# Kernel tuning notes

Hardware: AMD Instinct MI355X
Metric: run time of the kernel (lower is better)

Reference implementation:

```python
import jax, jax.numpy as jnp
import numpy as np

N_NODES = 50000
N_GRAPHS = 64
LRELU_SLOPE = 0.2
BN_EPS = 1e-5

def _conv1d(x, w, b):
    # x: [B, C_in, L], w: [C_out, C_in, K] -> [B, C_out, L-K+1]
    y = jax.lax.conv_general_dilated(x, w, window_strides=(1,), padding='VALID',
                                     dimension_numbers=('NCH', 'OIH', 'NCH'))
    return y + b[None, :, None]

def setup_inputs() -> dict:
    key = jax.random.key(0)
    ks = jax.random.split(key, 24)
    E = 800000
    inp = {
        'global_rna': jax.random.randint(ks[0], (64, 3000), 0, 5, dtype=jnp.int32),
        'local_rna': jax.random.randint(ks[1], (64, 2998), 0, 65, dtype=jnp.int32),
        'pro_x': jax.random.normal(ks[2], (N_NODES, 33), jnp.float32),
        'edge_index': jax.random.randint(ks[3], (2, E), 0, N_NODES, dtype=jnp.int32),
        'pro_weight': jax.random.uniform(ks[4], (E,), jnp.float32),
        'pro_batch': jnp.sort(jax.random.randint(ks[5], (N_NODES,), 0, N_GRAPHS, dtype=jnp.int32)),
        'emb1': jax.random.normal(ks[6], (5, 128), jnp.float32),
        'emb2': jax.random.normal(ks[7], (65, 128), jnp.float32),
        'conv1_w': jax.random.normal(ks[8], (32, 3000, 8), jnp.float32) * 0.02,
        'conv1_b': jax.random.normal(ks[9], (32,), jnp.float32) * 0.02,
        'conv2_w': jax.random.normal(ks[10], (32, 2998, 8), jnp.float32) * 0.02,
        'conv2_b': jax.random.normal(ks[11], (32,), jnp.float32) * 0.02,
        'fc_xr_w': jax.random.normal(ks[12], (128, 3872), jnp.float32) * 0.02,
        'fc_xr_b': jax.random.normal(ks[13], (128,), jnp.float32) * 0.02,
        'gcn_w': jax.random.normal(ks[14], (33, 33), jnp.float32) * 0.1,
        'gcn_b': jax.random.normal(ks[15], (33,), jnp.float32) * 0.1,
        'bn_mean': jnp.zeros((33,), jnp.float32),
        'bn_var': jnp.ones((33,), jnp.float32),
        'bn_weight': jnp.ones((33,), jnp.float32),
        'bn_bias': jnp.zeros((33,), jnp.float32),
        'gat_wl': jax.random.normal(ks[16], (132, 33), jnp.float32) * 0.1,
        'gat_wr': jax.random.normal(ks[17], (132, 33), jnp.float32) * 0.1,
        'gat_att': jax.random.normal(ks[18], (2, 66), jnp.float32) * 0.1,
        'gat_b': jax.random.normal(ks[19], (132,), jnp.float32) * 0.1,
        'fc1_w': jax.random.normal(ks[20], (1024, 132), jnp.float32) * 0.05,
        'fc1_b': jax.random.normal(ks[21], (1024,), jnp.float32) * 0.05,
        'fc2_w': jax.random.normal(ks[22], (128, 1024), jnp.float32) * 0.05,
        'fc2_b': jax.random.normal(ks[23], (128,), jnp.float32) * 0.05,
    }
    return inp

def _forward(global_rna, local_rna, pro_x, edge_index, pro_weight, pro_batch,
             emb1, emb2, conv1_w, conv1_b, conv2_w, conv2_b, fc_xr_w, fc_xr_b,
             gcn_w, gcn_b, bn_mean, bn_var, bn_weight, bn_bias,
             gat_wl, gat_wr, gat_att, gat_b, fc1_w, fc1_b, fc2_w, fc2_b):
    # ---- RNA global branch ----
    xrg = emb1[global_rna]                       # [B, 3000, 128]
    xrg = _conv1d(xrg, conv1_w, conv1_b)         # [B, 32, 121]
    xrg = xrg.reshape(-1, 32 * 121) @ fc_xr_w.T + fc_xr_b
    # ---- RNA local branch ----
    xrl = emb2[local_rna]                        # [B, 2998, 128]
    xrl = _conv1d(xrl, conv2_w, conv2_b)         # [B, 32, 121]
    xrl = xrl.reshape(-1, 32 * 121) @ fc_xr_w.T + fc_xr_b
    # ---- protein GCNConv (with self-loops, symmetric norm, edge weights) ----
    N = pro_x.shape[0]
    loop = jnp.arange(N, dtype=edge_index.dtype)
    src = jnp.concatenate([edge_index[0], loop])
    dst = jnp.concatenate([edge_index[1], loop])
    w = jnp.concatenate([pro_weight, jnp.ones((N,), pro_weight.dtype)])
    deg = jax.ops.segment_sum(w, dst, num_segments=N)
    dinv = jnp.where(deg > 0, jax.lax.rsqrt(deg), 0.0)
    norm = dinv[src] * w * dinv[dst]
    h = pro_x @ gcn_w.T                          # [N, 33]
    xp = jax.ops.segment_sum(h[src] * norm[:, None], dst, num_segments=N) + gcn_b
    xp = jax.nn.relu(xp)
    # ---- NodeLevelBatchNorm (eval: running stats) ----
    inv = bn_weight * jax.lax.rsqrt(bn_var + BN_EPS)
    xp = xp * inv + (bn_bias - bn_mean * inv)
    # ---- GATv2Conv (heads=2, out=66, concat, self-loops, eval: no dropout) ----
    H, C = 2, 66
    xl = (xp @ gat_wl.T).reshape(N, H, C)
    xr = (xp @ gat_wr.T).reshape(N, H, C)
    e = jnp.sum(jax.nn.leaky_relu(xl[src] + xr[dst], LRELU_SLOPE) * gat_att, axis=-1)  # [E2, H]
    emax = jax.ops.segment_max(e, dst, num_segments=N)                                  # [N, H]
    a = jnp.exp(e - emax[dst])
    asum = jax.ops.segment_sum(a, dst, num_segments=N)
    alpha = a / asum[dst]                                                              # [E2, H]
    xp = jax.ops.segment_sum(xl[src] * alpha[:, :, None], dst, num_segments=N)
    xp = xp.reshape(N, H * C) + gat_b
    xp = jax.nn.relu(xp)
    # ---- global mean pool ----
    cnt = jax.ops.segment_sum(jnp.ones((N,), xp.dtype), pro_batch, num_segments=N_GRAPHS)
    xp = jax.ops.segment_sum(xp, pro_batch, num_segments=N_GRAPHS) / jnp.maximum(cnt, 1.0)[:, None]
    # ---- protein MLP head (dropout = identity in eval) ----
    xp = jax.nn.relu(xp @ fc1_w.T + fc1_b)
    xp = xp @ fc2_w.T + fc2_b
    xc_rna = 0.5 * (xrg + xrl)
    return (xc_rna, xp)

def reference(global_rna, local_rna, pro_x, edge_index, pro_weight, pro_batch,
              emb1, emb2, conv1_w, conv1_b, conv2_w, conv2_b, fc_xr_w, fc_xr_b,
              gcn_w, gcn_b, bn_mean, bn_var, bn_weight, bn_bias,
              gat_wl, gat_wr, gat_att, gat_b, fc1_w, fc1_b, fc2_w, fc2_b):
    return _forward(global_rna, local_rna, pro_x, edge_index, pro_weight, pro_batch,
                    emb1, emb2, conv1_w, conv1_b, conv2_w, conv2_b, fc_xr_w, fc_xr_b,
                    gcn_w, gcn_b, bn_mean, bn_var, bn_weight, bn_bias,
                    gat_wl, gat_wr, gat_att, gat_b, fc1_w, fc1_b, fc2_w, fc2_b)
```

## Files before the change

kernel.cpp:

```cpp
#include <hip/hip_runtime.h>

#define N_NODES 50000
#define N_EDGES 800000
#define LRELU_SLOPE 0.2f
#define BN_EPS 1e-5f

typedef unsigned int u32;
typedef unsigned long long u64;

__device__ __forceinline__ float lrelu(float x){ return fmaxf(x,0.f) + LRELU_SLOPE*fminf(x,0.f); }
__device__ __forceinline__ float bflo(u32 u){ return __uint_as_float(u<<16); }
__device__ __forceinline__ float bfhi(u32 u){ return __uint_as_float(u & 0xffff0000u); }
__device__ __forceinline__ u32 packbf(float a, float b){
  u32 ua = __float_as_uint(a); ua = (ua + 0x7fffu + ((ua>>16)&1u)) >> 16;
  u32 ub = __float_as_uint(b); ub = (ub + 0x7fffu + ((ub>>16)&1u)) >> 16;
  return ua | (ub<<16);
}
__device__ __forceinline__ float degof(u64 p){
  return (float)(p & 0xFFFFFFFFFFull) * (1.0f/67108864.0f);
}

template<int CTRL>
__device__ __forceinline__ float dppadd(float x){
  int y = __builtin_amdgcn_update_dpp(0, __float_as_int(x), CTRL, 0xF, 0xF, false);
  return x + __int_as_float(y);
}
__device__ __forceinline__ float red8(float p){
  p = dppadd<0x141>(p);
  p = dppadd<0x4E>(p);
  p = dppadd<0xB1>(p);
  return p;
}
__device__ __forceinline__ float redall(float v){
  v = dppadd<0x128>(v);
  v += __shfl_xor(v, 16, 64);
  v += __shfl_xor(v, 32, 64);
  return v;
}

__global__ __launch_bounds__(256) void k_hist(const int* __restrict__ eidx, const float* __restrict__ pw,
                                              u64* __restrict__ pk){
  int e = blockIdx.x*256 + threadIdx.x;
  if(e < N_EDGES){
    int d = eidx[N_EDGES + e];
    u64 q = (u64)(pw[e] * 67108864.f);
    atomicAdd(&pk[d], (1ull<<40) | q);
  }
}

__global__ __launch_bounds__(256) void k_scan1(const u64* __restrict__ pk, int* __restrict__ rowptr,
                                               int* __restrict__ bsum){
  __shared__ int sc[256];
  int b = blockIdx.x, t = threadIdx.x;
  int i = b*256 + t;
  int v = (i < N_NODES) ? (int)(pk[i] >> 40) : 0;
  sc[t] = v;
  __syncthreads();
  for(int off=1; off<256; off<<=1){
    int x = (t>=off)? sc[t-off] : 0;
    __syncthreads();
    sc[t] += x;
    __syncthreads();
  }
  if(i < N_NODES) rowptr[i] = sc[t] - v;
  if(t == 255) bsum[b] = sc[255];
}

__global__ __launch_bounds__(256) void k_scan2(const int* __restrict__ bsum, int* __restrict__ bbase,
                                               int* __restrict__ rowptr, int* __restrict__ gstart,
                                               int* __restrict__ gend){
  __shared__ int sc[256];
  int t = threadIdx.x;
  int v = (t < 196) ? bsum[t] : 0;
  sc[t] = v;
  __syncthreads();
  for(int off=1; off<256; off<<=1){
    int x = (t>=off)? sc[t-off] : 0;
    __syncthreads();
    sc[t] += x;
    __syncthreads();
  }
  if(t < 196) bbase[t] = sc[t] - v;
  if(t == 255) rowptr[N_NODES] = sc[255];
  if(t < 64){ gstart[t] = N_NODES; gend[t] = 0; }
}

__global__ __launch_bounds__(256) void k_scan3(int* __restrict__ rowptr, const int* __restrict__ bbase){
  int b = blockIdx.x, t = threadIdx.x;
  int i = b*256 + t;
  if(i < N_NODES) rowptr[i] += bbase[b];
}

__global__ __launch_bounds__(256) void k_scatter(const int* __restrict__ eidx, const float* __restrict__ pw,
                                                 const int* __restrict__ rowptr, int* __restrict__ fill,
                                                 const u64* __restrict__ pk, uint2* __restrict__ s_srcw,
                                                 int* __restrict__ srcs){
  int e = blockIdx.x*256 + threadIdx.x;
  if(e < N_EDGES){
    int d = eidx[N_EDGES + e];
    int s = eidx[e];
    float ge = rsqrtf(degof(pk[s]) + 1.f) * pw[e];
    int pos = rowptr[d] + atomicAdd(&fill[d], 1);
    uint2 pr; pr.x = (u32)s; pr.y = __float_as_uint(ge);
    s_srcw[pos] = pr;
    srcs[pos] = s;
  }
}

__global__ __launch_bounds__(256) void k_h(const float* __restrict__ px, const float* __restrict__ gw,
                                           u32* __restrict__ hb){
  int n = blockIdx.x*256 + threadIdx.x;
  if(n >= N_NODES) return;
  float x[33];
  #pragma unroll
  for(int k=0;k<33;k++) x[k] = px[n*33+k];
  float a[33];
  for(int c=0;c<33;c++){
    float s = 0.f;
    #pragma unroll
    for(int k=0;k<33;k++) s = fmaf(x[k], gw[c*33+k], s);
    a[c] = s;
  }
  #pragma unroll
  for(int d=0;d<16;d++) hb[(size_t)n*17 + d] = packbf(a[2*d], a[2*d+1]);
  hb[(size_t)n*17 + 16] = packbf(a[32], 0.f);
}

__global__ __launch_bounds__(256) void k_gcn(const u32* __restrict__ hb, const int* __restrict__ rowptr,
                                             const uint2* __restrict__ s_srcw,
                                             const u64* __restrict__ pk,
                                             const float* __restrict__ gcnb, const float* __restrict__ bnm,
                                             const float* __restrict__ bnv, const float* __restrict__ bnw,
                                             const float* __restrict__ bnb, float* __restrict__ xp1){
  int wave = threadIdx.x >> 6;
  int lane = threadIdx.x & 63;
  int n = blockIdx.x*4 + wave;
  if(n >= N_NODES) return;
  int l = lane & 15, g = lane >> 4;
  bool t0 = (l == 0);
  float dn = rsqrtf(degof(pk[n]) + 1.f);
  const u32* srow = hb + (size_t)n*17;
  u32 us  = srow[l];
  u32 ust = t0 ? srow[16] : 0u;
  float acc0, acc1, acct;
  if(g == 0){ acc0 = dn*bflo(us); acc1 = dn*bfhi(us); acct = dn*bflo(ust); }
  else      { acc0 = 0.f; acc1 = 0.f; acct = 0.f; }
  int rb = rowptr[n], re = rowptr[n+1];
  int j = rb;
  for(; j+8 <= re; j += 8){
    uint2 prA = s_srcw[j + g];
    uint2 prB = s_srcw[j + 4 + g];
    float geA = __uint_as_float(prA.y);
    float geB = __uint_as_float(prB.y);
    const u32* rA = hb + (size_t)prA.x*17;
    const u32* rB = hb + (size_t)prB.x*17;
    u32 uA  = rA[l], uB = rB[l];
    u32 utA = t0 ? rA[16] : 0u;
    u32 utB = t0 ? rB[16] : 0u;
    acc0 = fmaf(geA, bflo(uA),  fmaf(geB, bflo(uB),  acc0));
    acc1 = fmaf(geA, bfhi(uA),  fmaf(geB, bfhi(uB),  acc1));
    acct = fmaf(geA, bflo(utA), fmaf(geB, bflo(utB), acct));
  }
  if(j+4 <= re){
    uint2 pr = s_srcw[j + g];
    float ge = __uint_as_float(pr.y);
    const u32* r = hb + (size_t)pr.x*17;
    u32 u  = r[l];
    u32 ut = t0 ? r[16] : 0u;
    acc0 = fmaf(ge, bflo(u),  acc0);
    acc1 = fmaf(ge, bfhi(u),  acc1);
    acct = fmaf(ge, bflo(ut), acct);
    j += 4;
  }
  int rem = re - j;
  if(rem > 0){
    bool val = (g < rem);
    uint2 pr = s_srcw[val ? (j + g) : j];
    float ge = val ? __uint_as_float(pr.y) : 0.f;
    const u32* r = hb + (size_t)pr.x*17;
    u32 u  = r[l];
    u32 ut = t0 ? r[16] : 0u;
    acc0 = fmaf(ge, bflo(u),  acc0);
    acc1 = fmaf(ge, bfhi(u),  acc1);
    acct = fmaf(ge, bflo(ut), acct);
  }
  #pragma unroll
  for(int m=16;m<=32;m<<=1){
    acc0 += __shfl_xor(acc0, m, 64);
    acc1 += __shfl_xor(acc1, m, 64);
    acct += __shfl_xor(acct, m, 64);
  }
  if(g == 0){
    int c0 = 2*l, c1 = 2*l+1;
    float v0 = fmaxf(dn*acc0 + gcnb[c0], 0.f);
    float v1 = fmaxf(dn*acc1 + gcnb[c1], 0.f);
    float i0 = bnw[c0] / sqrtf(bnv[c0] + BN_EPS);
    float i1 = bnw[c1] / sqrtf(bnv[c1] + BN_EPS);
    float2 o;
    o.x = v0*i0 + (bnb[c0] - bnm[c0]*i0);
    o.y = v1*i1 + (bnb[c1] - bnm[c1]*i1);
    ((float2*)(xp1 + (size_t)n*36))[l] = o;
    if(t0){
      float vt = fmaxf(dn*acct + gcnb[32], 0.f);
      float it = bnw[32] / sqrtf(bnv[32] + BN_EPS);
      float2 ot; ot.x = vt*it + (bnb[32] - bnm[32]*it); ot.y = 0.f;
      ((float2*)(xp1 + (size_t)n*36))[16] = ot;
      float2 z; z.x = 0.f; z.y = 0.f;
      ((float2*)(xp1 + (size_t)n*36))[17] = z;
    }
  }
}

__global__ __launch_bounds__(320) void k_gatlin(const float* __restrict__ xp1, const float* __restrict__ wl,
                                                const float* __restrict__ wr, const float* __restrict__ att,
                                                u32* __restrict__ xlb, float* __restrict__ xr){
  __shared__ float sx[64*36];
  __shared__ float swle[66*33];
  __shared__ float swlo[66*33];
  __shared__ float swre[66*33];
  __shared__ float swro[66*33];
  __shared__ float su[2][33];
  int t = threadIdx.x;
  int n0 = blockIdx.x*64;
  int nn = N_NODES - n0; if(nn > 64) nn = 64;
  for(int i=t;i<2178;i+=320){
    int d = i/33, k = i - d*33;
    int gb = d*66 + k;
    swle[i] = wl[gb];
    swlo[i] = wl[gb+33];
    swre[i] = wr[gb];
    swro[i] = wr[gb+33];
  }
  int xcnt = nn*36;
  for(int i=t;i<xcnt;i+=320) sx[i] = xp1[(size_t)n0*36 + i];
  __syncthreads();
  if(t < 66){
    int hh = (t >= 33) ? 1 : 0;
    int k = t - 33*hh;
    float s = 0.f;
    const float* ah = att + hh*66;
    #pragma unroll 3
    for(int dd=0;dd<33;dd++){
      int p = hh*33 + dd;
      s = fmaf(ah[2*dd],   swle[p*33+k], s);
      s = fmaf(ah[2*dd+1], swlo[p*33+k], s);
    }
    su[hh][k] = s;
  }
  if(t < 264){
    int ng = t/66, p = t - ng*66;
    int nbase = ng*16;
    float al0[16], al1[16], ar0[16], ar1[16];
    #pragma unroll
    for(int i=0;i<16;i++){ al0[i]=0.f; al1[i]=0.f; ar0[i]=0.f; ar1[i]=0.f; }
    const float* wle = swle + p*33;
    const float* wlo = swlo + p*33;
    const float* wre = swre + p*33;
    const float* wro = swro + p*33;
    for(int k=0;k<33;k++){
      float w0 = wle[k], w1 = wlo[k], w2 = wre[k], w3 = wro[k];
      const float* xcol = sx + nbase*36 + k;
      #pragma unroll
      for(int i=0;i<16;i++){
        float x = xcol[i*36];
        al0[i] = fmaf(x, w0, al0[i]);
        al1[i] = fmaf(x, w1, al1[i]);
        ar0[i] = fmaf(x, w2, ar0[i]);
        ar1[i] = fmaf(x, w3, ar1[i]);
      }
    }
    int head = (p >= 33) ? 1 : 0;
    int dd = p - 33*head;
    #pragma unroll
    for(int i=0;i<16;i++){
      int n = nbase + i;
      if(n < nn){
        size_t nidx = (size_t)(n0 + n);
        xlb[nidx*72 + head*36 + dd] = packbf(al0[i], al1[i]);
        float2 v; v.x = ar0[i]; v.y = ar1[i];
        ((float2*)xr)[nidx*66 + p] = v;
      }
    }
  }
  __syncthreads();
  if(t < 128){
    int nl = t >> 1, hh = t & 1;
    if(nl < nn){
      const float* xv = sx + nl*36;
      float s = 0.f;
      #pragma unroll
      for(int k=0;k<33;k++) s = fmaf(su[hh][k], xv[k], s);
      xlb[(size_t)(n0 + nl)*72 + hh*36 + 33] =
        __float_as_uint(s * (LRELU_SLOPE*1.44269504089f));
    }
  }
}

__global__ __launch_bounds__(128) void k_gat(const int* __restrict__ rowptr, const int* __restrict__ srcs,
                                             const u32* __restrict__ xlb, const float* __restrict__ xr,
                                             const float* __restrict__ att, const float* __restrict__ gatb,
                                             float* __restrict__ xp2){
  const float ATT_SC = (1.f - LRELU_SLOPE) * 1.44269504089f;
  int n = blockIdx.x;
  int h = threadIdx.x >> 6;
  int lane = threadIdx.x & 63;
  int l8 = lane & 7, g8 = lane >> 3;
  bool t0 = (l8 == 0);
  bool g0 = (g8 == 0);
  const float* xrp = xr + (size_t)n*132 + h*66 + 8*l8;
  float2 x01 = ((const float2*)xrp)[0];
  float2 x23 = ((const float2*)xrp)[1];
  float2 x45 = ((const float2*)xrp)[2];
  float2 x67 = ((const float2*)xrp)[3];
  float2 xt  = t0 ? *(const float2*)(xr + (size_t)n*132 + h*66 + 64) : make_float2(0.f,0.f);
  const float* ap = att + h*66 + 8*l8;
  float2 a01 = ((const float2*)ap)[0];
  float2 a23 = ((const float2*)ap)[1];
  float2 a45 = ((const float2*)ap)[2];
  float2 a67 = ((const float2*)ap)[3];
  a01.x *= ATT_SC; a01.y *= ATT_SC; a23.x *= ATT_SC; a23.y *= ATT_SC;
  a45.x *= ATT_SC; a45.y *= ATT_SC; a67.x *= ATT_SC; a67.y *= ATT_SC;
  float2 atl = *(const float2*)(att + h*66 + 64);
  atl.x *= ATT_SC; atl.y *= ATT_SC;

  const u32* xbase = xlb + h*36;
  float v0,v1,v2,v3,v4,v5,v6,v7,w0,w1;

#define GSCORE(U, TU, P) { \
  v0=bflo(U.x); v1=bfhi(U.x); v2=bflo(U.y); v3=bfhi(U.y); \
  v4=bflo(U.z); v5=bfhi(U.z); v6=bflo(U.w); v7=bfhi(U.w); \
  w0=bflo(TU.x); w1=bfhi(TU.x); \
  float pA = __uint_as_float(TU.y), pB = 0.f; \
  pA = fmaf(fmaxf(v0+x01.x,0.f), a01.x, pA); \
  pB = fmaf(fmaxf(v1+x01.y,0.f), a01.y, pB); \
  pA = fmaf(fmaxf(v2+x23.x,0.f), a23.x, pA); \
  pB = fmaf(fmaxf(v3+x23.y,0.f), a23.y, pB); \
  pA = fmaf(fmaxf(v4+x45.x,0.f), a45.x, pA); \
  pB = fmaf(fmaxf(v5+x45.y,0.f), a45.y, pB); \
  pA = fmaf(fmaxf(v6+x67.x,0.f), a67.x, pA); \
  pB = fmaf(fmaxf(v7+x67.y,0.f), a67.y, pB); \
  pA = fmaf(fmaxf(w0+xt.x,0.f), atl.x, pA); \
  pB = fmaf(fmaxf(w1+xt.y,0.f), atl.y, pB); \
  P = red8(pA + pB); }

  const u32* srow = xbase + (size_t)n*72;
  uint4 su = ((const uint4*)srow)[l8];
  uint2 stl = t0 ? ((const uint2*)srow)[16] : make_uint2(0u,0u);
  float ps;
  GSCORE(su, stl, ps);
  float cn = -ps;
  float A0 = g0? v0 : 0.f, A1 = g0? v1 : 0.f, A2 = g0? v2 : 0.f, A3 = g0? v3 : 0.f;
  float A4 = g0? v4 : 0.f, A5 = g0? v5 : 0.f, A6 = g0? v6 : 0.f, A7 = g0? v7 : 0.f;
  float T0 = g0? w0 : 0.f, T1 = g0? w1 : 0.f;
  float asum = g0 ? 1.f : 0.f;

  int rb = rowptr[n], re = rowptr[n+1];
  int j = rb;
  for(; j+8 <= re; j += 8){
    int s = srcs[j + g8];
    const u32* r = xbase + (size_t)s*72;
    uint4 u = ((const uint4*)r)[l8];
    uint2 tu = t0 ? ((const uint2*)r)[16] : make_uint2(0u,0u);
    float p;
    GSCORE(u, tu, p);
    float a = __builtin_amdgcn_exp2f(p + cn);
    A0 = fmaf(a, v0, A0); A1 = fmaf(a, v1, A1); A2 = fmaf(a, v2, A2); A3 = fmaf(a, v3, A3);
    A4 = fmaf(a, v4, A4); A5 = fmaf(a, v5, A5); A6 = fmaf(a, v6, A6); A7 = fmaf(a, v7, A7);
    T0 = fmaf(a, w0, T0); T1 = fmaf(a, w1, T1);
    asum += a;
  }
  int rem = re - j;
  if(rem > 0){
    bool val = (g8 < rem);
    int s = val ? srcs[j + g8] : n;
    const u32* r = xbase + (size_t)s*72;
    uint4 u = ((const uint4*)r)[l8];
    uint2 tu = t0 ? ((const uint2*)r)[16] : make_uint2(0u,0u);
    float p;
    GSCORE(u, tu, p);
    float a = val ? __builtin_amdgcn_exp2f(p + cn) : 0.f;
    A0 = fmaf(a, v0, A0); A1 = fmaf(a, v1, A1); A2 = fmaf(a, v2, A2); A3 = fmaf(a, v3, A3);
    A4 = fmaf(a, v4, A4); A5 = fmaf(a, v5, A5); A6 = fmaf(a, v6, A6); A7 = fmaf(a, v7, A7);
    T0 = fmaf(a, w0, T0); T1 = fmaf(a, w1, T1);
    asum += a;
  }
#undef GSCORE

  A0 = redall(A0); A1 = redall(A1); A2 = redall(A2); A3 = redall(A3);
  A4 = redall(A4); A5 = redall(A5); A6 = redall(A6); A7 = redall(A7);
  T0 = redall(T0); T1 = redall(T1);
  asum = redall(asum);

  if(g0){
    float inv = 1.f / asum;
    const float* gp = gatb + h*66 + 8*l8;
    float2 g01 = ((const float2*)gp)[0];
    float2 g23 = ((const float2*)gp)[1];
    float2 g45 = ((const float2*)gp)[2];
    float2 g67 = ((const float2*)gp)[3];
    float* op = xp2 + (size_t)n*132 + h*66 + 8*l8;
    float2 o;
    o.x = fmaxf(fmaf(A0,inv,g01.x),0.f); o.y = fmaxf(fmaf(A1,inv,g01.y),0.f); ((float2*)op)[0] = o;
    o.x = fmaxf(fmaf(A2,inv,g23.x),0.f); o.y = fmaxf(fmaf(A3,inv,g23.y),0.f); ((float2*)op)[1] = o;
    o.x = fmaxf(fmaf(A4,inv,g45.x),0.f); o.y = fmaxf(fmaf(A5,inv,g45.y),0.f); ((float2*)op)[2] = o;
    o.x = fmaxf(fmaf(A6,inv,g67.x),0.f); o.y = fmaxf(fmaf(A7,inv,g67.y),0.f); ((float2*)op)[3] = o;
    if(t0){
      float2 gt = *(const float2*)(gatb + h*66 + 64);
      float2 ot;
      ot.x = fmaxf(fmaf(T0,inv,gt.x),0.f); ot.y = fmaxf(fmaf(T1,inv,gt.y),0.f);
      *(float2*)(xp2 + (size_t)n*132 + h*66 + 64) = ot;
    }
  }
}

__global__ __launch_bounds__(256) void k_bounds(const int* __restrict__ batch, int* __restrict__ gstart,
                                                int* __restrict__ gend){
  int n = blockIdx.x*256 + threadIdx.x;
  if(n >= N_NODES) return;
  int b = batch[n];
  if(n == 0) gstart[b] = 0;
  else {
    int p = batch[n-1];
    if(p != b){ gstart[b] = n; gend[p] = n; }
  }
  if(n == N_NODES-1) gend[b] = N_NODES;
}

__global__ __launch_bounds__(128) void k_poolp(const float* __restrict__ xp2, const int* __restrict__ gstart,
                                               const int* __restrict__ gend, float* __restrict__ pp){
  int g = blockIdx.x, seg = blockIdx.y, t = threadIdx.x;
  int s = gstart[g], e = gend[g];
  int len = e - s; if(len < 0) len = 0;
  int ns = s + (int)(((long long)len*seg)>>4);
  int ne = s + (int)(((long long)len*(seg+1))>>4);
  float a0 = 0.f, a1 = 0.f;
  for(int n=ns;n<ne;n++){
    a0 += xp2[(size_t)n*132 + t];
    if(t < 4) a1 += xp2[(size_t)n*132 + 128 + t];
  }
  float* o = pp + (size_t)(g*16 + seg)*132;
  o[t] = a0;
  if(t < 4) o[128 + t] = a1;
}

__global__ __launch_bounds__(256) void k_pfc1(const float* __restrict__ pp, const int* __restrict__ gstart,
                                              const int* __restrict__ gend, const float* __restrict__ w,
                                              const float* __restrict__ b, float* __restrict__ h1T){
  __shared__ float pooled[132];
  int g = blockIdx.x, t = threadIdx.x;
  if(t < 132){
    float s = 0.f;
    #pragma unroll
    for(int k=0;k<16;k++) s += pp[(size_t)(g*16 + k)*132 + t];
    int c = gend[g] - gstart[g]; if(c < 1) c = 1;
    pooled[t] = s/(float)c;
  }
  __syncthreads();
  #pragma unroll
  for(int r=0;r<4;r++){
    int o = r*256 + t;
    const float* wr = w + o*132;
    float acc = b[o];
    for(int k=0;k<132;k++) acc = fmaf(pooled[k], wr[k], acc);
    h1T[o*64+g] = fmaxf(acc, 0.f);
  }
}

__global__ __launch_bounds__(256) void k_fc2(const float* __restrict__ h1T, const float* __restrict__ w,
                                             const float* __restrict__ b, float* __restrict__ out){
  __shared__ float part[256];
  int o = blockIdx.x, t = threadIdx.x;
  int s = t >> 6, g = t & 63;
  const float* wr = w + o*1024 + s*256;
  const float* hp = h1T + (size_t)(s*256)*64 + g;
  float acc = 0.f;
  for(int k=0;k<256;k++) acc = fmaf(hp[k*64], wr[k], acc);
  part[t] = acc;
  __syncthreads();
  if(s == 0){
    float r = b[o] + part[g] + part[64+g] + part[128+g] + part[192+g];
    out[8192 + g*128 + o] = r;
  }
}

__global__ __launch_bounds__(256) void k_bucket(const int* __restrict__ g, int L, int V,
                                                int* __restrict__ sci, int* __restrict__ off){
  __shared__ int gl[3000];
  __shared__ int hist[65];
  __shared__ int base[66];
  int b = blockIdx.x, t = threadIdx.x;
  if(t < V) hist[t] = 0;
  for(int i=t;i<L;i+=256) gl[i] = g[b*L + i];
  __syncthreads();
  for(int i=t;i<L;i+=256) atomicAdd(&hist[gl[i]], 1);
  __syncthreads();
  if(t == 0){
    int run = 0;
    for(int v=0;v<V;v++){ base[v] = run; run += hist[v]; }
    base[V] = run;
  }
  __syncthreads();
  if(t <= V) off[b*(V+1) + t] = base[t];
  if(t < V) hist[t] = 0;
  __syncthreads();
  for(int i=t;i<L;i+=256){
    int v = gl[i];
    int p = base[v] + atomicAdd(&hist[v], 1);
    sci[b*3000 + p] = i*8;
  }
}

__global__ __launch_bounds__(256) void k_sgather(const int* __restrict__ sci, const int* __restrict__ off,
                                                 const float* __restrict__ w, int V, int wstride,
                                                 int sstride, float* __restrict__ S){
  __shared__ int loff[66];
  __shared__ int lci[3000];
  int b = blockIdx.x, q = blockIdx.y, t = threadIdx.x;
  int nsplit = gridDim.y;
  if(t <= V) loff[t] = off[b*(V+1) + t];
  __syncthreads();
  int vs = (V*q)/nsplit, ve = (V*(q+1))/nsplit;
  if(vs == ve) return;
  int p0 = loff[vs], p1 = loff[ve];
  for(int i=p0+t;i<p1;i+=256) lci[i-p0] = sci[b*3000 + i];
  __syncthreads();
  int co = t >> 3, kk = t & 7;
  const float* wrow = w + co*wstride + kk;
  float* Srow = S + (size_t)b*32*sstride + co*sstride + kk;
  for(int v=vs;v<ve;v++){
    int j = loff[v] - p0, je = loff[v+1] - p0;
    float a0=0.f,a1=0.f,a2=0.f,a3=0.f,a4=0.f,a5=0.f,a6=0.f,a7=0.f;
    for(; j+8 <= je; j += 8){
      a0 += wrow[lci[j]];
      a1 += wrow[lci[j+1]];
      a2 += wrow[lci[j+2]];
      a3 += wrow[lci[j+3]];
      a4 += wrow[lci[j+4]];
      a5 += wrow[lci[j+5]];
      a6 += wrow[lci[j+6]];
      a7 += wrow[lci[j+7]];
    }
    for(; j<je; j++) a0 += wrow[lci[j]];
    Srow[v*8] = ((a0+a1)+(a2+a3)) + ((a4+a5)+(a6+a7));
  }
}

__global__ __launch_bounds__(128) void k_y(const float* __restrict__ S1, const float* __restrict__ S2,
                                           const float* __restrict__ emb1, const float* __restrict__ emb2,
                                           const float* __restrict__ c1b, const float* __restrict__ c2b,
                                           float* __restrict__ ysum){
  __shared__ float em1[640];
  __shared__ float em2[8320];
  __shared__ float Sa[320];
  __shared__ float Sb[4160];
  int b = blockIdx.x, cg = blockIdx.y, t = threadIdx.x;
  for(int i=t;i<640;i+=128)  em1[i] = emb1[i];
  for(int i=t;i<8320;i+=128) em2[i] = emb2[i];
  for(int i=t;i<320;i+=128)  Sa[i] = S1[b*1280 + cg*320 + i];
  for(int i=t;i<4160;i+=128) Sb[i] = S2[(size_t)b*16640 + cg*4160 + i];
  __syncthreads();
  if(t >= 121) return;
  #pragma unroll
  for(int c8=0;c8<8;c8++){
    int co = cg*8 + c8;
    const float* sa = Sa + c8*40;
    float acc1 = c1b[co];
    #pragma unroll
    for(int v=0;v<5;v++)
      #pragma unroll
      for(int k=0;k<8;k++) acc1 = fmaf(sa[v*8+k], em1[v*128 + t + k], acc1);
    const float* sb = Sb + c8*520;
    float acc2 = c2b[co];
    for(int v=0;v<65;v++){
      #pragma unroll
      for(int k=0;k<8;k++) acc2 = fmaf(sb[v*8+k], em2[v*128 + t + k], acc2);
    }
    ysum[b*3872 + co*121 + t] = 0.5f*(acc1 + acc2);
  }
}

__global__ __launch_bounds__(256) void k_fcxr(const float* __restrict__ ysum, const float* __restrict__ fcw,
                                              const float* __restrict__ fcb, float* __restrict__ out){
  __shared__ float part[512];
  int bp = blockIdx.x, q = blockIdx.y, t = threadIdx.x;
  int b0 = bp*2;
  int ol = t >> 3;
  int o  = q*32 + ol;
  int slice = t & 7;
  const float4* ys0 = (const float4*)(ysum + b0*3872) + slice*121;
  const float4* ys1 = (const float4*)(ysum + (b0+1)*3872) + slice*121;
  const float4* wr  = (const float4*)(fcw + (size_t)o*3872) + slice*121;
  float acc0 = 0.f, acc1 = 0.f;
  for(int k=0;k<121;k++){
    float4 w4 = wr[k];
    float4 y0 = ys0[k], y1 = ys1[k];
    acc0 += y0.x*w4.x + y0.y*w4.y + y0.z*w4.z + y0.w*w4.w;
    acc1 += y1.x*w4.x + y1.y*w4.y + y1.z*w4.z + y1.w*w4.w;
  }
  part[t] = acc0;
  part[256+t] = acc1;
  __syncthreads();
  if(slice == 0){
    float s0 = fcb[o], s1 = fcb[o];
    #pragma unroll
    for(int i=0;i<8;i++){ s0 += part[ol*8 + i]; s1 += part[256 + ol*8 + i]; }
    out[b0*128 + o] = s0;
    out[(b0+1)*128 + o] = s1;
  }
}

extern "C" void kernel_launch(void* const* d_in, const int* in_sizes, int n_in,
                              void* d_out, int out_size, void* d_ws, size_t ws_size,
                              hipStream_t stream){
  const int*   g_rna = (const int*)  d_in[0];
  const int*   l_rna = (const int*)  d_in[1];
  const float* pro_x = (const float*)d_in[2];
  const int*   eidx  = (const int*)  d_in[3];
  const float* pro_w = (const float*)d_in[4];
  const int*   batch = (const int*)  d_in[5];
  const float* emb1  = (const float*)d_in[6];
  const float* emb2  = (const float*)d_in[7];
  const float* c1w   = (const float*)d_in[8];
  const float* c1b   = (const float*)d_in[9];
  const float* c2w   = (const float*)d_in[10];
  const float* c2b   = (const float*)d_in[11];
  const float* fcxw  = (const float*)d_in[12];
  const float* fcxb  = (const float*)d_in[13];
  const float* gcnw  = (const float*)d_in[14];
  const float* gcnb  = (const float*)d_in[15];
  const float* bnm   = (const float*)d_in[16];
  const float* bnv   = (const float*)d_in[17];
  const float* bnw   = (const float*)d_in[18];
  const float* bnb   = (const float*)d_in[19];
  const float* gwl   = (const float*)d_in[20];
  const float* gwr   = (const float*)d_in[21];
  const float* gatt  = (const float*)d_in[22];
  const float* gatb  = (const float*)d_in[23];
  const float* f1w   = (const float*)d_in[24];
  const float* f1b   = (const float*)d_in[25];
  const float* f2w   = (const float*)d_in[26];
  const float* f2b_  = (const float*)d_in[27];
  float* out = (float*)d_out;

  char* ws = (char*)d_ws;
  size_t off = 0;
  auto A = [&](size_t n)->char*{ char* p = ws + off; off = (off + n + 255) & ~(size_t)255; return p; };
  u64*   pk     = (u64*)  A((size_t)N_NODES*8);
  int*   fill   = (int*)  A((size_t)N_NODES*4);
  size_t zero_bytes = off;
  int*   rowptr = (int*)  A((size_t)(N_NODES+1)*4);
  int*   bsum   = (int*)  A(196*4);
  int*   bbase  = (int*)  A(196*4);
  uint2* s_srcw = (uint2*)A((size_t)N_EDGES*8);
  int*   srcs   = (int*)  A((size_t)N_EDGES*4);
  u32*   hb     = (u32*)  A((size_t)N_NODES*17*4);
  float* xp1    = (float*)A((size_t)N_NODES*36*4);
  u32*   xlb    = (u32*)  A((size_t)N_NODES*72*4);
  float* xr     = (float*)A((size_t)N_NODES*132*4);
  float* xp2    = (float*)A((size_t)N_NODES*132*4);
  int*   gstart = (int*)  A(64*4);
  int*   gend   = (int*)  A(64*4);
  float* pp     = (float*)A((size_t)64*16*132*4);
  float* h1T    = (float*)A(1024*64*4);
  float* S1     = (float*)A((size_t)64*1280*4);
  float* S2     = (float*)A((size_t)64*16640*4);
  float* ysum   = (float*)A((size_t)64*3872*4);
  int*   sci1   = (int*)  A((size_t)64*3000*4);
  int*   off1   = (int*)  A((size_t)64*8*4);
  int*   sci2   = (int*)  A((size_t)64*3000*4);
  int*   off2   = (int*)  A((size_t)64*66*4);
  (void)ws_size; (void)in_sizes; (void)n_in; (void)out_size;

  hipMemsetAsync(ws, 0, zero_bytes, stream);

  k_hist   <<<3125, 256, 0, stream>>>(eidx, pro_w, pk);
  k_scan1  <<<196, 256, 0, stream>>>(pk, rowptr, bsum);
  k_scan2  <<<1, 256, 0, stream>>>(bsum, bbase, rowptr, gstart, gend);
  k_scan3  <<<196, 256, 0, stream>>>(rowptr, bbase);
  k_scatter<<<3125, 256, 0, stream>>>(eidx, pro_w, rowptr, fill, pk, s_srcw, srcs);
  k_h      <<<196, 256, 0, stream>>>(pro_x, gcnw, hb);
  k_gcn    <<<12500, 256, 0, stream>>>(hb, rowptr, s_srcw, pk, gcnb, bnm, bnv, bnw, bnb, xp1);
  k_gatlin <<<782, 320, 0, stream>>>(xp1, gwl, gwr, gatt, xlb, xr);
  k_gat    <<<N_NODES, 128, 0, stream>>>(rowptr, srcs, xlb, xr, gatt, gatb, xp2);
  k_bounds <<<196, 256, 0, stream>>>(batch, gstart, gend);
  k_poolp  <<<dim3(64,16), 128, 0, stream>>>(xp2, gstart, gend, pp);
  k_pfc1   <<<64, 256, 0, stream>>>(pp, gstart, gend, f1w, f1b, h1T);
  k_fc2    <<<128, 256, 0, stream>>>(h1T, f2w, f2b_, out);

  k_bucket <<<64, 256, 0, stream>>>(g_rna, 3000, 5, sci1, off1);
  k_bucket <<<64, 256, 0, stream>>>(l_rna, 2998, 65, sci2, off2);
  k_sgather<<<dim3(64,5), 256, 0, stream>>>(sci1, off1, c1w, 5, 24000, 40, S1);
  k_sgather<<<dim3(64,32), 256, 0, stream>>>(sci2, off2, c2w, 65, 23984, 520, S2);
  k_y      <<<dim3(64,4), 128, 0, stream>>>(S1, S2, emb1, emb2, c1b, c2b, ysum);
  k_fcxr   <<<dim3(32,4), 256, 0, stream>>>(ysum, fcxw, fcxb, out);
}
```

Before: 560.7 us.

## Bin edges by destination block before CSR placement to localize scattered writes

Replaces the single scatter pass with two passes. The first pass appends each edge to a coarse bucket keyed by its destination block (128 nodes), stored in a scratch buffer that aliases the later xr array, and overflow edges fall back to direct placement. The second pass runs one block per bucket and places edges into CSR order, which is meant to make the scattered writes and the per-node fill atomics more local and cache-friendly. It also drops the separate srcs array; the GAT kernel reads source indices from the interleaved s_srcw pairs instead, which adds an extra pass and bucket atomic contention in exchange.

After: 814.6 us. 45.3% more time.

```diff
diff --git a/kernel.cpp b/kernel.cpp
--- a/kernel.cpp
+++ b/kernel.cpp
@@ -4,6 +4,10 @@
 #define N_EDGES 800000
 #define LRELU_SLOPE 0.2f
 #define BN_EPS 1e-5f
+
+#define BSHIFT 7
+#define NBUCK 391
+#define BCAP 4096
 
 typedef unsigned int u32;
 typedef unsigned long long u64;
@@ -91,19 +95,39 @@
   if(i < N_NODES) rowptr[i] += bbase[b];
 }
 
-__global__ __launch_bounds__(256) void k_scatter(const int* __restrict__ eidx, const float* __restrict__ pw,
-                                                 const int* __restrict__ rowptr, int* __restrict__ fill,
-                                                 const u64* __restrict__ pk, uint2* __restrict__ s_srcw,
-                                                 int* __restrict__ srcs){
+__global__ __launch_bounds__(256) void k_bin(const int* __restrict__ eidx, const float* __restrict__ pw,
+                                             const u64* __restrict__ pk, const int* __restrict__ rowptr,
+                                             int* __restrict__ fill, int* __restrict__ bcnt,
+                                             uint4* __restrict__ ebuf, uint2* __restrict__ s_srcw){
   int e = blockIdx.x*256 + threadIdx.x;
-  if(e < N_EDGES){
-    int d = eidx[N_EDGES + e];
-    int s = eidx[e];
-    float ge = rsqrtf(degof(pk[s]) + 1.f) * pw[e];
+  if(e >= N_EDGES) return;
+  int d = eidx[N_EDGES + e];
+  int s = eidx[e];
+  float ge = rsqrtf(degof(pk[s]) + 1.f) * pw[e];
+  int b = d >> BSHIFT;
+  int slot = atomicAdd(&bcnt[b], 1);
+  if(slot < BCAP){
+    uint4 r; r.x = (u32)s; r.y = __float_as_uint(ge); r.z = (u32)d; r.w = 0u;
+    ebuf[(size_t)b*BCAP + slot] = r;
+  } else {
     int pos = rowptr[d] + atomicAdd(&fill[d], 1);
     uint2 pr; pr.x = (u32)s; pr.y = __float_as_uint(ge);
     s_srcw[pos] = pr;
-    srcs[pos] = s;
+  }
+}
+
+__global__ __launch_bounds__(256) void k_place(const int* __restrict__ bcnt, const uint4* __restrict__ ebuf,
+                                               const int* __restrict__ rowptr, int* __restrict__ fill,
+                                               uint2* __restrict__ s_srcw){
+  int b = blockIdx.x;
+  int cnt = bcnt[b]; if(cnt > BCAP) cnt = BCAP;
+  const uint4* eb = ebuf + (size_t)b*BCAP;
+  for(int i=threadIdx.x; i<cnt; i+=256){
+    uint4 r = eb[i];
+    int d = (int)r.z;
+    int pos = rowptr[d] + atomicAdd(&fill[d], 1);
+    uint2 pr; pr.x = r.x; pr.y = r.y;
+    s_srcw[pos] = pr;
   }
 }
 
@@ -296,7 +320,7 @@
   }
 }
 
-__global__ __launch_bounds__(128) void k_gat(const int* __restrict__ rowptr, const int* __restrict__ srcs,
+__global__ __launch_bounds__(128) void k_gat(const int* __restrict__ rowptr, const u32* __restrict__ srcx,
                                              const u32* __restrict__ xlb, const float* __restrict__ xr,
                                              const float* __restrict__ att, const float* __restrict__ gatb,
                                              float* __restrict__ xp2){
@@ -357,7 +381,7 @@
   int rb = rowptr[n], re = rowptr[n+1];
   int j = rb;
   for(; j+8 <= re; j += 8){
-    int s = srcs[j + g8];
+    int s = (int)srcx[2*(j + g8)];
     const u32* r = xbase + (size_t)s*72;
     uint4 u = ((const uint4*)r)[l8];
     uint2 tu = t0 ? ((const uint2*)r)[16] : make_uint2(0u,0u);
@@ -372,7 +396,7 @@
   int rem = re - j;
   if(rem > 0){
     bool val = (g8 < rem);
-    int s = val ? srcs[j + g8] : n;
+    int s = val ? (int)srcx[2*(j + g8)] : n;
     const u32* r = xbase + (size_t)s*72;
     uint4 u = ((const uint4*)r)[l8];
     uint2 tu = t0 ? ((const uint2*)r)[16] : make_uint2(0u,0u);
@@ -647,12 +671,12 @@
   auto A = [&](size_t n)->char*{ char* p = ws + off; off = (off + n + 255) & ~(size_t)255; return p; };
   u64*   pk     = (u64*)  A((size_t)N_NODES*8);
   int*   fill   = (int*)  A((size_t)N_NODES*4);
+  int*   bcnt   = (int*)  A((size_t)NBUCK*4);
   size_t zero_bytes = off;
   int*   rowptr = (int*)  A((size_t)(N_NODES+1)*4);
   int*   bsum   = (int*)  A(196*4);
   int*   bbase  = (int*)  A(196*4);
   uint2* s_srcw = (uint2*)A((size_t)N_EDGES*8);
-  int*   srcs   = (int*)  A((size_t)N_EDGES*4);
   u32*   hb     = (u32*)  A((size_t)N_NODES*17*4);
   float* xp1    = (float*)A((size_t)N_NODES*36*4);
   u32*   xlb    = (u32*)  A((size_t)N_NODES*72*4);
@@ -671,17 +695,20 @@
   int*   off2   = (int*)  A((size_t)64*66*4);
   (void)ws_size; (void)in_sizes; (void)n_in; (void)out_size;
 
+  uint4* ebuf = (uint4*)xr;
+
   hipMemsetAsync(ws, 0, zero_bytes, stream);
 
   k_hist   <<<3125, 256, 0, stream>>>(eidx, pro_w, pk);
   k_scan1  <<<196, 256, 0, stream>>>(pk, rowptr, bsum);
   k_scan2  <<<1, 256, 0, stream>>>(bsum, bbase, rowptr, gstart, gend);
   k_scan3  <<<196, 256, 0, stream>>>(rowptr, bbase);
-  k_scatter<<<3125, 256, 0, stream>>>(eidx, pro_w, rowptr, fill, pk, s_srcw, srcs);
+  k_bin    <<<3125, 256, 0, stream>>>(eidx, pro_w, pk, rowptr, fill, bcnt, ebuf, s_srcw);
+  k_place  <<<NBUCK, 256, 0, stream>>>(bcnt, ebuf, rowptr, fill, s_srcw);
   k_h      <<<196, 256, 0, stream>>>(pro_x, gcnw, hb);
   k_gcn    <<<12500, 256, 0, stream>>>(hb, rowptr, s_srcw, pk, gcnb, bnm, bnv, bnw, bnb, xp1);
   k_gatlin <<<782, 320, 0, stream>>>(xp1, gwl, gwr, gatt, xlb, xr);
-  k_gat    <<<N_NODES, 128, 0, stream>>>(rowptr, srcs, xlb, xr, gatt, gatb, xp2);
+  k_gat    <<<N_NODES, 128, 0, stream>>>(rowptr, (const u32*)s_srcw, xlb, xr, gatt, gatb, xp2);
   k_bounds <<<196, 256, 0, stream>>>(batch, gstart, gend);
   k_poolp  <<<dim3(64,16), 128, 0, stream>>>(xp2, gstart, gend, pp);
   k_pfc1   <<<64, 256, 0, stream>>>(pp, gstart, gend, f1w, f1b, h1T);
```
